# Performance work log

Measured on AMD Instinct MI355X. Metric: run time of the kernel, lower is better.

## Reference

```python
import jax, jax.numpy as jnp
import numpy as np

EPS = 1e-10

def setup_inputs() -> dict:
    key = jax.random.key(0)
    k1, k2, k3 = jax.random.split(key, 3)
    B, R, S, C = 4, 4096, 96, 32
    colors = jax.random.uniform(k1, (B, R, S, C), dtype=jnp.float32)
    densities = jax.random.normal(k2, (B, R, S, 1), dtype=jnp.float32)
    # depths: sorted increasing along the sample axis, in a plausible near/far range
    depths = jnp.sort(jax.random.uniform(k3, (B, R, S, 1), dtype=jnp.float32) * 1.8 + 0.8, axis=2)
    return {"colors": colors, "densities": densities, "depths": depths}

def reference(colors, densities, depths):
    # clamp_mode == 'softplus', white_back == False, foreground-only path
    deltas = depths[:, :, 1:] - depths[:, :, :-1]                      # [B,R,S-1,1]
    colors_mid = (colors[:, :, :-1] + colors[:, :, 1:]) * 0.5          # [B,R,S-1,C]
    densities_mid = (densities[:, :, :-1] + densities[:, :, 1:]) * 0.5
    depths_mid = (depths[:, :, :-1] + depths[:, :, 1:]) * 0.5

    densities_mid = jax.nn.softplus(densities_mid - 1.0)
    density_delta = densities_mid * deltas
    alpha = 1.0 - jnp.exp(-density_delta)                              # [B,R,S-1,1]

    ones = jnp.ones_like(alpha[:, :, :1])
    alpha_shifted = jnp.concatenate([ones, 1.0 - alpha + EPS], axis=-2)  # [B,R,S,1]
    transmittance = jnp.cumprod(alpha_shifted, axis=-2)                # per-ray scan
    weights = alpha * transmittance[:, :, :-1]                         # [B,R,S-1,1]
    weight_bg = transmittance[:, :, -1][..., None]                     # [B,R,1,1]

    composite_rgb = jnp.sum(weights * colors_mid, axis=-2)             # [B,R,C]
    weight_total = jnp.sum(weights, axis=2)                            # [B,R,1]
    composite_depth = jnp.sum(weights * depths_mid, axis=-2) / weight_total
    composite_depth = jnp.where(jnp.isnan(composite_depth), jnp.inf, composite_depth)
    composite_depth = jnp.clip(composite_depth, jnp.min(depths), jnp.max(depths))

    composite_rgb = composite_rgb * 2.0 - 1.0
    return composite_rgb, composite_depth, weights, alpha, weight_bg
```

## Files before the change

### kernel.cpp

```cpp
#include <hip/hip_runtime.h>
#include <math.h>

#define NS 96
#define SM1 95
#define NC 32
#define REPS 1e-10f

__global__ __launch_bounds__(256) void raymarch_scan(
    const float* __restrict__ densities,
    const float* __restrict__ depths,
    float* __restrict__ out_depth,
    float* __restrict__ out_w,
    float* __restrict__ out_alpha,
    float* __restrict__ out_wbg,
    float* __restrict__ ws_coeff,
    float* __restrict__ ws_d0,
    float* __restrict__ ws_d1)
{
    const int ray  = blockIdx.x * 4 + (threadIdx.x >> 6);
    const int lane = threadIdx.x & 63;

    const float* dep = depths + (size_t)ray * NS;
    const float* den = densities + (size_t)ray * NS;

    const int i1 = 64 + lane;
    float dep0 = dep[lane];
    float den0 = den[lane];
    float dep1 = (i1 < NS) ? dep[i1] : 0.0f;
    float den1 = (i1 < NS) ? den[i1] : 0.0f;

    float dn0 = __shfl(dep0, (lane + 1) & 63);
    float en0 = __shfl(den0, (lane + 1) & 63);
    float d64 = __shfl(dep1, 0);
    float e64 = __shfl(den1, 0);
    if (lane == 63) { dn0 = d64; en0 = e64; }
    float dn1 = __shfl(dep1, (lane + 1) & 63);
    float en1 = __shfl(den1, (lane + 1) & 63);

    float dm0  = 0.5f * (den0 + en0) - 1.0f;
    float sp0  = fmaxf(dm0, 0.0f) + __logf(1.0f + __expf(-fabsf(dm0)));
    float a0   = 1.0f - __expf(-sp0 * (dn0 - dep0));
    float mid0 = 0.5f * (dep0 + dn0);

    float a1 = 0.0f, mid1 = 0.0f;
    if (lane < 31) {
        float dm1 = 0.5f * (den1 + en1) - 1.0f;
        float sp1 = fmaxf(dm1, 0.0f) + __logf(1.0f + __expf(-fabsf(dm1)));
        a1   = 1.0f - __expf(-sp1 * (dn1 - dep1));
        mid1 = 0.5f * (dep1 + dn1);
    }

    float oma0 = 1.0f - a0 + REPS;
    float oma1 = (lane < 31) ? (1.0f - a1 + REPS) : 1.0f;

    float x = oma0;
    #pragma unroll
    for (int off = 1; off < 64; off <<= 1) {
        float v = __shfl_up(x, off);
        if (lane >= off) x *= v;
    }
    float total0 = __shfl(x, 63);

    float y = oma1;
    #pragma unroll
    for (int off = 1; off < 64; off <<= 1) {
        float v = __shfl_up(y, off);
        if (lane >= off) y *= v;
    }

    float xs = __shfl_up(x, 1);
    float T0 = (lane == 0) ? 1.0f : xs;
    float w0 = a0 * T0;
    float ys = __shfl_up(y, 1);
    float T1 = ((lane == 0) ? 1.0f : ys) * total0;
    float w1 = a1 * T1;

    float wbg = __shfl(y, 30) * total0;

    float w0p = __shfl_up(w0, 1);
    float c0  = 0.5f * (((lane == 0) ? 0.0f : w0p) + w0);
    float w1p = __shfl_up(w1, 1);
    float w63 = __shfl(w0, 63);
    float c1  = 0.5f * (((lane == 0) ? w63 : w1p) + w1);

    float wsum = w0 + w1;
    float dsum = w0 * mid0 + ((lane < 31) ? w1 * mid1 : 0.0f);
    #pragma unroll
    for (int off = 32; off > 0; off >>= 1) {
        wsum += __shfl_xor(wsum, off);
        dsum += __shfl_xor(dsum, off);
    }

    const size_t b95 = (size_t)ray * SM1;
    const size_t b96 = (size_t)ray * NS;
    out_alpha[b95 + lane] = a0;
    out_w[b95 + lane]     = w0;
    ws_coeff[b96 + lane]  = c0;
    if (lane < 31) {
        out_alpha[b95 + 64 + lane] = a1;
        out_w[b95 + 64 + lane]     = w1;
    }
    if (lane < 32) {
        ws_coeff[b96 + 64 + lane] = c1;
    }
    float dlast = __shfl(dep1, 31);
    if (lane == 0) {
        out_wbg[ray] = wbg;
        float cd = dsum / wsum;
        if (cd != cd) cd = __builtin_inff();
        out_depth[ray] = cd;
        ws_d0[ray] = dep0;
        ws_d1[ray] = dlast;
    }
}

__global__ __launch_bounds__(256) void raymarch_color(
    const float* __restrict__ colors,
    const float* __restrict__ ws_coeff,
    float* __restrict__ out_rgb)
{
    const int t  = threadIdx.x;
    const int r0 = blockIdx.x * 16;

    __shared__ float s_coeff[16 * 97];

    #pragma unroll
    for (int k = 0; k < 6; ++k) {
        int i = t + k * 256;
        int r = i / NS, s = i - r * NS;
        s_coeff[r * 97 + s] = ws_coeff[(size_t)(r0 + r) * NS + s];
    }
    __syncthreads();

    const int g = t & 7;
    const int h = (t >> 3) & 1;
    const int rl = t >> 4;
    const int ray = r0 + rl;
    const int sbase = h * 48;

    const float4* col4 = (const float4*)(colors + (size_t)ray * NS * NC);
    const float* cf = &s_coeff[rl * 97 + sbase];

    float4 acc = {0.0f, 0.0f, 0.0f, 0.0f};
    #pragma unroll 12
    for (int i = 0; i < 48; ++i) {
        float4 v = col4[(sbase + i) * 8 + g];
        float c = cf[i];
        acc.x = fmaf(c, v.x, acc.x);
        acc.y = fmaf(c, v.y, acc.y);
        acc.z = fmaf(c, v.z, acc.z);
        acc.w = fmaf(c, v.w, acc.w);
    }

    acc.x += __shfl_xor(acc.x, 8);
    acc.y += __shfl_xor(acc.y, 8);
    acc.z += __shfl_xor(acc.z, 8);
    acc.w += __shfl_xor(acc.w, 8);

    if (h == 0) {
        float4 o;
        o.x = 2.0f * acc.x - 1.0f;
        o.y = 2.0f * acc.y - 1.0f;
        o.z = 2.0f * acc.z - 1.0f;
        o.w = 2.0f * acc.w - 1.0f;
        ((float4*)(out_rgb + (size_t)ray * NC))[g] = o;
    }
}

__global__ __launch_bounds__(256) void raymarch_finalize(
    const float* __restrict__ ws_d0,
    const float* __restrict__ ws_d1,
    float* __restrict__ out_depth,
    int rays)
{
    __shared__ float s_mn[256];
    __shared__ float s_mx[256];
    const int tid = threadIdx.x;

    float mn = __builtin_inff();
    float mx = -__builtin_inff();
    for (int r = tid; r < rays; r += 256) {
        mn = fminf(mn, ws_d0[r]);
        mx = fmaxf(mx, ws_d1[r]);
    }
    s_mn[tid] = mn;
    s_mx[tid] = mx;
    __syncthreads();
    for (int off = 128; off > 0; off >>= 1) {
        if (tid < off) {
            s_mn[tid] = fminf(s_mn[tid], s_mn[tid + off]);
            s_mx[tid] = fmaxf(s_mx[tid], s_mx[tid + off]);
        }
        __syncthreads();
    }
    const float dmin = s_mn[0];
    const float dmax = s_mx[0];

    const int r = blockIdx.x * 256 + tid;
    if (r < rays) {
        float cd = out_depth[r];
        cd = fminf(fmaxf(cd, dmin), dmax);
        out_depth[r] = cd;
    }
}

extern "C" void kernel_launch(void* const* d_in, const int* in_sizes, int n_in,
                              void* d_out, int out_size, void* d_ws, size_t ws_size,
                              hipStream_t stream) {
    const float* colors    = (const float*)d_in[0];
    const float* densities = (const float*)d_in[1];
    const float* depths    = (const float*)d_in[2];

    const int rays = in_sizes[2] / NS;

    float* out = (float*)d_out;
    float* out_rgb   = out;
    float* out_depth = out_rgb + (size_t)rays * NC;
    float* out_w     = out_depth + rays;
    float* out_alpha = out_w + (size_t)rays * SM1;
    float* out_wbg   = out_alpha + (size_t)rays * SM1;

    float* ws       = (float*)d_ws;
    float* ws_d0    = ws;
    float* ws_d1    = ws + rays;
    float* ws_coeff = ws + 2 * (size_t)rays;

    raymarch_scan<<<rays / 4, 256, 0, stream>>>(
        densities, depths,
        out_depth, out_w, out_alpha, out_wbg, ws_coeff, ws_d0, ws_d1);

    raymarch_color<<<rays / 16, 256, 0, stream>>>(colors, ws_coeff, out_rgb);

    raymarch_finalize<<<(rays + 255) / 256, 256, 0, stream>>>(
        ws_d0, ws_d1, out_depth, rays);
}
```

Before: 315.9 us.

## Fuse color compositing into the scan kernel and prefetch colors into registers

Merges the color accumulation kernel into the per-ray scan kernel, so the per-sample coefficients are passed between lanes by shuffles instead of going through a global workspace buffer and shared memory. Each wavefront issues its 12 float4 color loads at kernel start, so their latency overlaps the transmittance scan. This removes one kernel launch and a write and re-read of the coefficient buffer. In exchange, each thread holds 48 more registers, which may lower occupancy, and the cross-lane reduction grows to three shuffle rounds per component.

```diff
diff --git a/kernel.cpp b/kernel.cpp
--- a/kernel.cpp
+++ b/kernel.cpp
@@ -6,19 +6,27 @@
 #define NC 32
 #define REPS 1e-10f
 
-__global__ __launch_bounds__(256) void raymarch_scan(
+__global__ __launch_bounds__(256) void raymarch_fused(
+    const float* __restrict__ colors,
     const float* __restrict__ densities,
     const float* __restrict__ depths,
+    float* __restrict__ out_rgb,
     float* __restrict__ out_depth,
     float* __restrict__ out_w,
     float* __restrict__ out_alpha,
     float* __restrict__ out_wbg,
-    float* __restrict__ ws_coeff,
     float* __restrict__ ws_d0,
     float* __restrict__ ws_d1)
 {
     const int ray  = blockIdx.x * 4 + (threadIdx.x >> 6);
     const int lane = threadIdx.x & 63;
+
+    const float4* col4 = (const float4*)(colors + (size_t)ray * NS * NC);
+    float4 v[12];
+    #pragma unroll
+    for (int k = 0; k < 12; ++k) {
+        v[k] = col4[lane + 64 * k];
+    }
 
     const float* dep = depths + (size_t)ray * NS;
     const float* den = densities + (size_t)ray * NS;
@@ -56,16 +64,16 @@
     float x = oma0;
     #pragma unroll
     for (int off = 1; off < 64; off <<= 1) {
-        float v = __shfl_up(x, off);
-        if (lane >= off) x *= v;
+        float vv = __shfl_up(x, off);
+        if (lane >= off) x *= vv;
     }
     float total0 = __shfl(x, 63);
 
     float y = oma1;
     #pragma unroll
     for (int off = 1; off < 64; off <<= 1) {
-        float v = __shfl_up(y, off);
-        if (lane >= off) y *= v;
+        float vv = __shfl_up(y, off);
+        if (lane >= off) y *= vv;
     }
 
     float xs = __shfl_up(x, 1);
@@ -92,16 +100,11 @@
     }
 
     const size_t b95 = (size_t)ray * SM1;
-    const size_t b96 = (size_t)ray * NS;
     out_alpha[b95 + lane] = a0;
     out_w[b95 + lane]     = w0;
-    ws_coeff[b96 + lane]  = c0;
     if (lane < 31) {
         out_alpha[b95 + 64 + lane] = a1;
         out_w[b95 + 64 + lane]     = w1;
-    }
-    if (lane < 32) {
-        ws_coeff[b96 + 64 + lane] = c1;
     }
     float dlast = __shfl(dep1, 31);
     if (lane == 0) {
@@ -112,58 +115,41 @@
         ws_d0[ray] = dep0;
         ws_d1[ray] = dlast;
     }
-}
-
-__global__ __launch_bounds__(256) void raymarch_color(
-    const float* __restrict__ colors,
-    const float* __restrict__ ws_coeff,
-    float* __restrict__ out_rgb)
-{
-    const int t  = threadIdx.x;
-    const int r0 = blockIdx.x * 16;
-
-    __shared__ float s_coeff[16 * 97];
-
-    #pragma unroll
-    for (int k = 0; k < 6; ++k) {
-        int i = t + k * 256;
-        int r = i / NS, s = i - r * NS;
-        s_coeff[r * 97 + s] = ws_coeff[(size_t)(r0 + r) * NS + s];
-    }
-    __syncthreads();
-
-    const int g = t & 7;
-    const int h = (t >> 3) & 1;
-    const int rl = t >> 4;
-    const int ray = r0 + rl;
-    const int sbase = h * 48;
-
-    const float4* col4 = (const float4*)(colors + (size_t)ray * NS * NC);
-    const float* cf = &s_coeff[rl * 97 + sbase];
-
+
+    const int srow = lane >> 3;
     float4 acc = {0.0f, 0.0f, 0.0f, 0.0f};
-    #pragma unroll 12
-    for (int i = 0; i < 48; ++i) {
-        float4 v = col4[(sbase + i) * 8 + g];
-        float c = cf[i];
-        acc.x = fmaf(c, v.x, acc.x);
-        acc.y = fmaf(c, v.y, acc.y);
-        acc.z = fmaf(c, v.z, acc.z);
-        acc.w = fmaf(c, v.w, acc.w);
-    }
-
-    acc.x += __shfl_xor(acc.x, 8);
-    acc.y += __shfl_xor(acc.y, 8);
-    acc.z += __shfl_xor(acc.z, 8);
-    acc.w += __shfl_xor(acc.w, 8);
-
-    if (h == 0) {
+    #pragma unroll
+    for (int k = 0; k < 8; ++k) {
+        float c = __shfl(c0, srow + 8 * k);
+        acc.x = fmaf(c, v[k].x, acc.x);
+        acc.y = fmaf(c, v[k].y, acc.y);
+        acc.z = fmaf(c, v[k].z, acc.z);
+        acc.w = fmaf(c, v[k].w, acc.w);
+    }
+    #pragma unroll
+    for (int k = 8; k < 12; ++k) {
+        float c = __shfl(c1, srow + 8 * (k - 8));
+        acc.x = fmaf(c, v[k].x, acc.x);
+        acc.y = fmaf(c, v[k].y, acc.y);
+        acc.z = fmaf(c, v[k].z, acc.z);
+        acc.w = fmaf(c, v[k].w, acc.w);
+    }
+
+    #pragma unroll
+    for (int m = 8; m < 64; m <<= 1) {
+        acc.x += __shfl_xor(acc.x, m);
+        acc.y += __shfl_xor(acc.y, m);
+        acc.z += __shfl_xor(acc.z, m);
+        acc.w += __shfl_xor(acc.w, m);
+    }
+
+    if (lane < 8) {
         float4 o;
         o.x = 2.0f * acc.x - 1.0f;
         o.y = 2.0f * acc.y - 1.0f;
         o.z = 2.0f * acc.z - 1.0f;
         o.w = 2.0f * acc.w - 1.0f;
-        ((float4*)(out_rgb + (size_t)ray * NC))[g] = o;
+        ((float4*)(out_rgb + (size_t)ray * NC))[lane] = o;
     }
 }
 
@@ -220,16 +206,13 @@
     float* out_alpha = out_w + (size_t)rays * SM1;
     float* out_wbg   = out_alpha + (size_t)rays * SM1;
 
-    float* ws       = (float*)d_ws;
-    float* ws_d0    = ws;
-    float* ws_d1    = ws + rays;
-    float* ws_coeff = ws + 2 * (size_t)rays;
-
-    raymarch_scan<<<rays / 4, 256, 0, stream>>>(
-        densities, depths,
-        out_depth, out_w, out_alpha, out_wbg, ws_coeff, ws_d0, ws_d1);
-
-    raymarch_color<<<rays / 16, 256, 0, stream>>>(colors, ws_coeff, out_rgb);
+    float* ws    = (float*)d_ws;
+    float* ws_d0 = ws;
+    float* ws_d1 = ws + rays;
+
+    raymarch_fused<<<rays / 4, 256, 0, stream>>>(
+        colors, densities, depths,
+        out_rgb, out_depth, out_w, out_alpha, out_wbg, ws_d0, ws_d1);
 
     raymarch_finalize<<<(rays + 255) / 256, 256, 0, stream>>>(
         ws_d0, ws_d1, out_depth, rays);
```

After: 302.5 us. -4.3%, faster.
